# Optimization experiments

Measured on AMD Instinct MI355X. Metric: run time of the kernel, lower is better.

The kernel has to match this reference:

```python
import jax, jax.numpy as jnp
import numpy as np

jax.config.update("jax_enable_x64", True)

TOL = 1e-06


def setup_inputs() -> dict:
    key = jax.random.key(0)
    k1, k2 = jax.random.split(key)
    n, d = 4096, 128
    output = jax.random.normal(k1, (n, d), dtype=jnp.float32)
    # target: square roots of patristic distances -> nonnegative
    target = jax.random.uniform(k2, (n, n), dtype=jnp.float32) * 2.0
    return {"output": output, "target": target}


def reference(output, target):
    # Torch module casts to double before all math
    out = output.astype(jnp.float64)
    tgt = target.astype(jnp.float64)
    n = out.shape[0]

    # Lorentz inner product: B = outer(s, s) - out @ out.T, s = sqrt(1 + ||o||^2)
    s = jnp.sqrt(1.0 + jnp.sum(out * out, axis=1))          # [n]
    B = s[:, None] * s[None, :] - out @ out.T               # [n, n]

    # Clamp near-1 entries exactly to 1 (torch: B[(B-1).abs() < tol] = 1.0)
    clamp = jnp.abs(B - 1.0) < TOL
    # Safe acosh: evaluate at 2.0 where clamped to avoid inf/nan, then set dist=0 there
    B_safe = jnp.where(clamp, 2.0, B)
    dist = jnp.where(clamp, 0.0, jnp.arccosh(B_safe))       # acosh(1) == 0

    # Strictly-lower-triangular masked MAE
    tril_mask = jnp.tril(jnp.ones((n, n), dtype=jnp.float64), k=-1)
    loss = jnp.sum(jnp.abs(dist - tgt) * tril_mask) / (n * (n - 1))
    return loss
```

## Files before the change

### kernel.cpp

```cpp
#include <hip/hip_runtime.h>
#include <math.h>

#define N 4096
#define D 128
#define TS 64
#define NT (N / TS)
#define NBLK (NT * (NT + 1) / 2)
#define NG (N / 16)
#define TPAD 68

typedef __attribute__((ext_vector_type(8))) short short8;
typedef __attribute__((ext_vector_type(4))) float f32x4;

union frag_u { short8 v; unsigned int u[4]; };

__device__ __forceinline__ unsigned int pack_bf16x2(float a, float b) {
    unsigned int ua = __float_as_uint(a), ub = __float_as_uint(b);
    ua = (ua + 0x7FFFu + ((ua >> 16) & 1u)) >> 16;
    ub = (ub + 0x7FFFu + ((ub >> 16) & 1u)) >> 16;
    return ua | (ub << 16);
}

__global__ __launch_bounds__(256)
void prep_kernel(const float* __restrict__ O,
                 short8* __restrict__ Ofrag,
                 float* __restrict__ s) {
    __shared__ float psum[16][17];
    const int g    = blockIdx.x;
    const int tid  = threadIdx.x;
    const int kk   = tid >> 6;
    const int lane = tid & 63;
    const int r16  = lane & 15;
    const int qd   = lane >> 4;
    const float* src = O + (size_t)(g * 16 + r16) * D + kk * 32 + qd * 8;
    const float4 v0 = *(const float4*)(src);
    const float4 v1 = *(const float4*)(src + 4);
    frag_u f;
    f.u[0] = pack_bf16x2(v0.x, v0.y);
    f.u[1] = pack_bf16x2(v0.z, v0.w);
    f.u[2] = pack_bf16x2(v1.x, v1.y);
    f.u[3] = pack_bf16x2(v1.z, v1.w);
    Ofrag[(g * 4 + kk) * 64 + lane] = f.v;
    psum[kk * 4 + qd][r16] = v0.x * v0.x + v0.y * v0.y + v0.z * v0.z + v0.w * v0.w
                           + v1.x * v1.x + v1.y * v1.y + v1.z * v1.z + v1.w * v1.w;
    __syncthreads();
    if (tid < 16) {
        float acc = 1.0f;
        #pragma unroll
        for (int x = 0; x < 16; x++) acc += psum[x][tid];
        s[g * 16 + tid] = sqrtf(acc);
    }
}

__device__ __forceinline__ float acosh_dist(float B) {
    if (fabsf(B - 1.0f) < 1e-6f) return 0.0f;
    const float Bc = fmaxf(B, 1.0f);
    return __log2f(Bc + sqrtf(fmaf(Bc, Bc, -1.0f))) * 0.6931471805599453f;
}

__global__ __launch_bounds__(256, 4)
void tile_loss_kernel(const short8* __restrict__ Fr,
                      const float* __restrict__ s,
                      const float* __restrict__ tgt,
                      float* __restrict__ partials) {
    __shared__ float T[TS][TPAD];
    __shared__ float wsum[4];

    const int t = blockIdx.x;
    int ti = (int)((sqrtf(8.0f * (float)t + 1.0f) - 1.0f) * 0.5f);
    while ((ti + 1) * (ti + 2) / 2 <= t) ti++;
    while (ti * (ti + 1) / 2 > t) ti--;
    const int tj = t - ti * (ti + 1) / 2;

    const int tid  = threadIdx.x;
    const int wave = tid >> 6;
    const int lane = tid & 63;
    const int quad = lane >> 4;
    const int l16  = lane & 15;

    const int ib0 = ti * TS;
    const int jb  = tj * TS;

    {
        const int r = tid >> 4;
        const int c = (tid & 15) * 4;
        float4 tg[4];
        #pragma unroll
        for (int p = 0; p < 4; p++)
            tg[p] = *(const float4*)(tgt + (size_t)(ib0 + p * 16 + r) * N + jb + c);
        #pragma unroll
        for (int p = 0; p < 4; p++)
            *(float4*)&T[p * 16 + r][c] = tg[p];
    }

    float sj[4];
    #pragma unroll
    for (int n = 0; n < 4; n++) sj[n] = s[jb + n * 16 + l16];
    const int r0 = wave * 16 + quad * 4;
    float si[4];
    #pragma unroll
    for (int r = 0; r < 4; r++) si[r] = s[ib0 + r0 + r];

    f32x4 acc[4] = {};
    const int ga4 = (ti * 4 + wave) * 4;
    const int gb4 = tj * 4 * 4;
    #pragma unroll
    for (int kp = 0; kp < 2; kp++) {
        const int k0 = kp * 2, k1 = kp * 2 + 1;
        const short8 a0 = Fr[(ga4 + k0) * 64 + lane];
        const short8 a1 = Fr[(ga4 + k1) * 64 + lane];
        short8 b0[4], b1[4];
        #pragma unroll
        for (int n = 0; n < 4; n++) {
            b0[n] = Fr[(gb4 + n * 4 + k0) * 64 + lane];
            b1[n] = Fr[(gb4 + n * 4 + k1) * 64 + lane];
        }
        #pragma unroll
        for (int n = 0; n < 4; n++)
            acc[n] = __builtin_amdgcn_mfma_f32_16x16x32_bf16(a0, b0[n], acc[n], 0, 0, 0);
        #pragma unroll
        for (int n = 0; n < 4; n++)
            acc[n] = __builtin_amdgcn_mfma_f32_16x16x32_bf16(a1, b1[n], acc[n], 0, 0, 0);
    }

    __syncthreads();

    float lsum = 0.0f;
    if (ti != tj) {
        #pragma unroll
        for (int r = 0; r < 4; r++)
            #pragma unroll
            for (int n = 0; n < 4; n++) {
                const float B  = fmaf(si[r], sj[n], -acc[n][r]);
                const float tv = T[r0 + r][n * 16 + l16];
                lsum += fabsf(acosh_dist(B) - tv);
            }
    } else {
        #pragma unroll
        for (int r = 0; r < 4; r++) {
            const int i = ib0 + r0 + r;
            #pragma unroll
            for (int n = 0; n < 4; n++) {
                const int j = jb + n * 16 + l16;
                if (j < i) {
                    const float B  = fmaf(si[r], sj[n], -acc[n][r]);
                    const float tv = T[r0 + r][n * 16 + l16];
                    lsum += fabsf(acosh_dist(B) - tv);
                }
            }
        }
    }

    #pragma unroll
    for (int off = 32; off > 0; off >>= 1)
        lsum += __shfl_down(lsum, off, 64);
    if (lane == 0) wsum[wave] = lsum;
    __syncthreads();
    if (tid == 0)
        partials[t] = wsum[0] + wsum[1] + wsum[2] + wsum[3];
}

__global__ __launch_bounds__(256)
void final_reduce_kernel(const float* __restrict__ partials,
                         float* __restrict__ loss) {
    __shared__ float wsum[4];
    const int tid  = threadIdx.x;
    const int wave = tid >> 6;
    const int lane = tid & 63;
    float acc = 0.0f;
    for (int i = tid; i < NBLK; i += 256) acc += partials[i];
    #pragma unroll
    for (int off = 32; off > 0; off >>= 1)
        acc += __shfl_down(acc, off, 64);
    if (lane == 0) wsum[wave] = acc;
    __syncthreads();
    if (tid == 0) {
        const float tot = wsum[0] + wsum[1] + wsum[2] + wsum[3];
        loss[0] = tot * (1.0f / ((float)N * (float)(N - 1)));
    }
}

extern "C" void kernel_launch(void* const* d_in, const int* in_sizes, int n_in,
                              void* d_out, int out_size, void* d_ws, size_t ws_size,
                              hipStream_t stream) {
    const float* O   = (const float*)d_in[0];
    const float* tgt = (const float*)d_in[1];
    float* loss = (float*)d_out;

    short8* Ofrag = (short8*)d_ws;
    float* s        = (float*)((char*)d_ws + (size_t)N * D * 2);
    float* partials = s + N;

    prep_kernel<<<NG, 256, 0, stream>>>(O, Ofrag, s);
    tile_loss_kernel<<<NBLK, 256, 0, stream>>>(Ofrag, s, tgt, partials);
    final_reduce_kernel<<<1, 256, 0, stream>>>(partials, loss);
}
```

Before: 102.0 us.

## Fuse final reduction via last-block atomic counter and load targets into registers

Removes the separate final_reduce kernel launch. Each tile block atomically increments a counter, and the last block to finish sums all partials and writes the loss. The target tile is now read straight into registers in the MFMA output layout, which drops the shared-memory staging and one barrier. The trade-off is that the direct target loads are 64-byte row segments per lane group rather than coalesced float4 loads, and the tail block does the serial reduction.

```diff
diff --git a/kernel.cpp b/kernel.cpp
--- a/kernel.cpp
+++ b/kernel.cpp
@@ -7,7 +7,6 @@
 #define NT (N / TS)
 #define NBLK (NT * (NT + 1) / 2)
 #define NG (N / 16)
-#define TPAD 68
 
 typedef __attribute__((ext_vector_type(8))) short short8;
 typedef __attribute__((ext_vector_type(4))) float f32x4;
@@ -24,10 +23,12 @@
 __global__ __launch_bounds__(256)
 void prep_kernel(const float* __restrict__ O,
                  short8* __restrict__ Ofrag,
-                 float* __restrict__ s) {
+                 float* __restrict__ s,
+                 unsigned int* __restrict__ done) {
     __shared__ float psum[16][17];
     const int g    = blockIdx.x;
     const int tid  = threadIdx.x;
+    if (g == 0 && tid == 0) *done = 0u;
     const int kk   = tid >> 6;
     const int lane = tid & 63;
     const int r16  = lane & 15;
@@ -62,9 +63,11 @@
 void tile_loss_kernel(const short8* __restrict__ Fr,
                       const float* __restrict__ s,
                       const float* __restrict__ tgt,
-                      float* __restrict__ partials) {
-    __shared__ float T[TS][TPAD];
+                      float* __restrict__ partials,
+                      unsigned int* __restrict__ done,
+                      float* __restrict__ loss) {
     __shared__ float wsum[4];
+    __shared__ int lastFlag;
 
     const int t = blockIdx.x;
     int ti = (int)((sqrtf(8.0f * (float)t + 1.0f) - 1.0f) * 0.5f);
@@ -80,23 +83,19 @@
 
     const int ib0 = ti * TS;
     const int jb  = tj * TS;
+    const int r0  = wave * 16 + quad * 4;
 
-    {
-        const int r = tid >> 4;
-        const int c = (tid & 15) * 4;
-        float4 tg[4];
+    float tv[4][4];
+    #pragma unroll
+    for (int r = 0; r < 4; r++) {
+        const float* trow = tgt + (size_t)(ib0 + r0 + r) * N + jb + l16;
         #pragma unroll
-        for (int p = 0; p < 4; p++)
-            tg[p] = *(const float4*)(tgt + (size_t)(ib0 + p * 16 + r) * N + jb + c);
-        #pragma unroll
-        for (int p = 0; p < 4; p++)
-            *(float4*)&T[p * 16 + r][c] = tg[p];
+        for (int n = 0; n < 4; n++) tv[r][n] = trow[n * 16];
     }
 
     float sj[4];
     #pragma unroll
     for (int n = 0; n < 4; n++) sj[n] = s[jb + n * 16 + l16];
-    const int r0 = wave * 16 + quad * 4;
     float si[4];
     #pragma unroll
     for (int r = 0; r < 4; r++) si[r] = s[ib0 + r0 + r];
@@ -123,17 +122,14 @@
             acc[n] = __builtin_amdgcn_mfma_f32_16x16x32_bf16(a1, b1[n], acc[n], 0, 0, 0);
     }
 
-    __syncthreads();
-
     float lsum = 0.0f;
     if (ti != tj) {
         #pragma unroll
         for (int r = 0; r < 4; r++)
             #pragma unroll
             for (int n = 0; n < 4; n++) {
-                const float B  = fmaf(si[r], sj[n], -acc[n][r]);
-                const float tv = T[r0 + r][n * 16 + l16];
-                lsum += fabsf(acosh_dist(B) - tv);
+                const float B = fmaf(si[r], sj[n], -acc[n][r]);
+                lsum += fabsf(acosh_dist(B) - tv[r][n]);
             }
     } else {
         #pragma unroll
@@ -143,9 +139,8 @@
             for (int n = 0; n < 4; n++) {
                 const int j = jb + n * 16 + l16;
                 if (j < i) {
-                    const float B  = fmaf(si[r], sj[n], -acc[n][r]);
-                    const float tv = T[r0 + r][n * 16 + l16];
-                    lsum += fabsf(acosh_dist(B) - tv);
+                    const float B = fmaf(si[r], sj[n], -acc[n][r]);
+                    lsum += fabsf(acosh_dist(B) - tv[r][n]);
                 }
             }
         }
@@ -156,27 +151,27 @@
         lsum += __shfl_down(lsum, off, 64);
     if (lane == 0) wsum[wave] = lsum;
     __syncthreads();
-    if (tid == 0)
-        partials[t] = wsum[0] + wsum[1] + wsum[2] + wsum[3];
-}
 
-__global__ __launch_bounds__(256)
-void final_reduce_kernel(const float* __restrict__ partials,
-                         float* __restrict__ loss) {
-    __shared__ float wsum[4];
-    const int tid  = threadIdx.x;
-    const int wave = tid >> 6;
-    const int lane = tid & 63;
-    float acc = 0.0f;
-    for (int i = tid; i < NBLK; i += 256) acc += partials[i];
-    #pragma unroll
-    for (int off = 32; off > 0; off >>= 1)
-        acc += __shfl_down(acc, off, 64);
-    if (lane == 0) wsum[wave] = acc;
+    if (tid == 0) {
+        const float p = wsum[0] + wsum[1] + wsum[2] + wsum[3];
+        __hip_atomic_store(&partials[t], p, __ATOMIC_RELAXED, __HIP_MEMORY_SCOPE_AGENT);
+        const unsigned int old =
+            __hip_atomic_fetch_add(done, 1u, __ATOMIC_ACQ_REL, __HIP_MEMORY_SCOPE_AGENT);
+        lastFlag = (old == (unsigned int)(NBLK - 1)) ? 1 : 0;
+    }
     __syncthreads();
-    if (tid == 0) {
-        const float tot = wsum[0] + wsum[1] + wsum[2] + wsum[3];
-        loss[0] = tot * (1.0f / ((float)N * (float)(N - 1)));
+    if (lastFlag) {
+        float acc2 = 0.0f;
+        for (int i = tid; i < NBLK; i += 256)
+            acc2 += __hip_atomic_load(&partials[i], __ATOMIC_RELAXED, __HIP_MEMORY_SCOPE_AGENT);
+        #pragma unroll
+        for (int off = 32; off > 0; off >>= 1)
+            acc2 += __shfl_down(acc2, off, 64);
+        if (lane == 0) wsum[wave] = acc2;
+        __syncthreads();
+        if (tid == 0)
+            loss[0] = (wsum[0] + wsum[1] + wsum[2] + wsum[3])
+                    * (1.0f / ((float)N * (float)(N - 1)));
     }
 }
 
@@ -190,8 +185,8 @@
     short8* Ofrag = (short8*)d_ws;
     float* s        = (float*)((char*)d_ws + (size_t)N * D * 2);
     float* partials = s + N;
+    unsigned int* done = (unsigned int*)(partials + NBLK);
 
-    prep_kernel<<<NG, 256, 0, stream>>>(O, Ofrag, s);
-    tile_loss_kernel<<<NBLK, 256, 0, stream>>>(Ofrag, s, tgt, partials);
-    final_reduce_kernel<<<1, 256, 0, stream>>>(partials, loss);
+    prep_kernel<<<NG, 256, 0, stream>>>(O, Ofrag, s, done);
+    tile_loss_kernel<<<NBLK, 256, 0, stream>>>(Ofrag, s, tgt, partials, done, loss);
 }
```

Result: slower. 154.8 us (+51.8%).
